# Performance work log

Measured on AMD Instinct MI355X. Metric: run time of the kernel, lower is better.

The kernel has to match this reference:

```python
import jax, jax.numpy as jnp
import numpy as np

HEAD_SIZE = 128
N_EMBD = 64
B, T = 8, 4096


def setup_inputs() -> dict:
    key = jax.random.key(0)
    k1, k2, k3, k4 = jax.random.split(key, 4)
    x = jax.random.normal(k1, (B, T, N_EMBD), dtype=jnp.float32)
    Wq = jax.random.normal(k2, (N_EMBD, HEAD_SIZE), dtype=jnp.float32) * (N_EMBD ** -0.5)
    Wk = jax.random.normal(k3, (N_EMBD, HEAD_SIZE), dtype=jnp.float32) * (N_EMBD ** -0.5)
    Wv = jax.random.normal(k4, (N_EMBD, HEAD_SIZE), dtype=jnp.float32) * (N_EMBD ** -0.5)
    return {"x": x, "Wq": Wq, "Wk": Wk, "Wv": Wv}


def reference(x, Wq, Wk, Wv):
    # x: [B, T, C]; single-head causal self-attention (nanoGPT Head)
    q = x @ Wq  # [B, T, H]
    k = x @ Wk  # [B, T, H]
    v = x @ Wv  # [B, T, H]
    scale = HEAD_SIZE ** -0.5
    scores = jnp.einsum("bth,bsh->bts", q, k) * scale  # [B, T, T]
    t = x.shape[1]
    causal = jnp.tril(jnp.ones((t, t), dtype=bool))  # [T, T]
    scores = jnp.where(causal[None, :, :], scores, jnp.float32(-jnp.inf))
    wei = jax.nn.softmax(scores, axis=-1)  # [B, T, T]; dropout p=0.0 -> identity
    out = jnp.einsum("bts,bsh->bth", wei, v)  # [B, T, H]
    return out
```

## Files before the change

### kernel.cpp

```cpp
#include <hip/hip_runtime.h>
#include <math.h>

#define BB 8
#define TT 4096
#define CC 64
#define HH 128
#define NTH 256
#define XSTR 72
#define WSTR 72
#define QSCALE ((float)(0.08838834764831845 * 1.4426950408889634))

typedef __attribute__((ext_vector_type(8)))  short short8;
typedef __attribute__((ext_vector_type(4)))  float floatx4;
typedef __attribute__((ext_vector_type(16))) float floatx16;

__device__ __forceinline__ unsigned short f2bf(float f) {
    union { float f; unsigned int u; } un; un.f = f;
    unsigned int r = un.u + 0x7FFF + ((un.u >> 16) & 1);
    return (unsigned short)(r >> 16);
}
__device__ __forceinline__ unsigned int pack2bf_fast(float a, float b) {
    union { float f; unsigned int u; } ua, ub; ua.f = a; ub.f = b;
    return __builtin_amdgcn_perm(ub.u + 0x8000u, ua.u + 0x8000u, 0x07060302u);
}
__device__ __forceinline__ float bflo(unsigned int u) {
    union { unsigned int u; float f; } x; x.u = u << 16; return x.f;
}
__device__ __forceinline__ float bfhi(unsigned int u) {
    union { unsigned int u; float f; } x; x.u = u & 0xffff0000u; return x.f;
}

__global__ __launch_bounds__(NTH) void qkv_mfma(
    const float* __restrict__ x,
    const float* __restrict__ Wq, const float* __restrict__ Wk, const float* __restrict__ Wv,
    unsigned short* __restrict__ qb, unsigned short* __restrict__ Kf,
    unsigned short* __restrict__ Vf)
{
    __shared__ __align__(16) unsigned short xs[64 * XSTR];
    __shared__ __align__(16) unsigned short Wts[3 * HH * WSTR];

    const int tid  = threadIdx.x;
    const int w    = tid >> 6;
    const int lane = tid & 63;
    const int quad = lane >> 4;
    const int lr   = lane & 15;

    const int b    = blockIdx.x >> 6;
    const int kblk = blockIdx.x & 63;
    const int t0   = kblk * 64;
    const long long rbase = (long long)b * TT + t0;

#pragma unroll
    for (int i = 0; i < 4; ++i) {
        const int idx = tid + i * NTH;
        const int r = idx >> 4, c4 = idx & 15;
        const float4 v = *(const float4*)(x + (rbase + r) * CC + c4 * 4);
        unsigned short tmp[4] = { f2bf(v.x), f2bf(v.y), f2bf(v.z), f2bf(v.w) };
        *(unsigned long long*)&xs[r * XSTR + c4 * 4] = *(unsigned long long*)tmp;
    }
#pragma unroll
    for (int mat = 0; mat < 3; ++mat) {
        const float* W = mat == 0 ? Wq : (mat == 1 ? Wk : Wv);
        const float s = mat == 0 ? QSCALE : 1.0f;
#pragma unroll
        for (int i = 0; i < 32; ++i) {
            const int idx = tid + i * NTH;
            const int c = idx >> 7, h = idx & 127;
            Wts[(mat * HH + h) * WSTR + c] = f2bf(W[idx] * s);
        }
    }
    __syncthreads();

    const short8 bx0 = *(const short8*)&xs[(w * 16 + lr) * XSTR + quad * 8];
    const short8 bx1 = *(const short8*)&xs[(w * 16 + lr) * XSTR + 32 + quad * 8];

    {
        const unsigned short* Wrow = Wts;
#pragma unroll
        for (int ht = 0; ht < 8; ++ht) {
            const short8 aw0 = *(const short8*)(Wrow + (ht * 16 + lr) * WSTR + quad * 8);
            const short8 aw1 = *(const short8*)(Wrow + (ht * 16 + lr) * WSTR + 32 + quad * 8);
            floatx4 acc = (floatx4)0.f;
            acc = __builtin_amdgcn_mfma_f32_16x16x32_bf16(aw0, bx0, acc, 0, 0, 0);
            acc = __builtin_amdgcn_mfma_f32_16x16x32_bf16(aw1, bx1, acc, 0, 0, 0);
            ushort4 st = { f2bf(acc[0]), f2bf(acc[1]), f2bf(acc[2]), f2bf(acc[3]) };
            *(ushort4*)(qb + (rbase + w * 16 + lr) * HH + ht * 16 + quad * 4) = st;
        }
    }
    {
        const unsigned short* Wrow = Wts + 1 * HH * WSTR;
        const int khp = w >> 1;
        const int lqp = (w & 1) * 16 + lr;
        unsigned short* kdst = Kf + ((long long)((b * 64 + kblk) * 2 + khp)) * 4096
                             + ((quad >> 1) & 1) * 256 + lqp * 8 + (quad & 1) * 4;
#pragma unroll
        for (int ht = 0; ht < 8; ++ht) {
            const short8 aw0 = *(const short8*)(Wrow + (ht * 16 + lr) * WSTR + quad * 8);
            const short8 aw1 = *(const short8*)(Wrow + (ht * 16 + lr) * WSTR + 32 + quad * 8);
            floatx4 acc = (floatx4)0.f;
            acc = __builtin_amdgcn_mfma_f32_16x16x32_bf16(aw0, bx0, acc, 0, 0, 0);
            acc = __builtin_amdgcn_mfma_f32_16x16x32_bf16(aw1, bx1, acc, 0, 0, 0);
            ushort4 st = { f2bf(acc[0]), f2bf(acc[1]), f2bf(acc[2]), f2bf(acc[3]) };
            *(ushort4*)(kdst + ht * 512) = st;
        }
    }
    {
        const unsigned short* Wrow = Wts + 2 * HH * WSTR;
        const int khv = w >> 1, ksv = w & 1, lsv = (quad >> 1) & 1;
        unsigned short* vdst = Vf + (long long)(b * 64 + kblk) * 8192 + khv * 4096
                             + ksv * 512 + lsv * 256 + (quad & 1) * 4;
#pragma unroll
        for (int htp = 0; htp < 8; ++htp) {
            const short8 bw0 = *(const short8*)(Wrow + (htp * 16 + lr) * WSTR + quad * 8);
            const short8 bw1 = *(const short8*)(Wrow + (htp * 16 + lr) * WSTR + 32 + quad * 8);
            floatx4 acc = (floatx4)0.f;
            acc = __builtin_amdgcn_mfma_f32_16x16x32_bf16(bx0, bw0, acc, 0, 0, 0);
            acc = __builtin_amdgcn_mfma_f32_16x16x32_bf16(bx1, bw1, acc, 0, 0, 0);
            ushort4 st = { f2bf(acc[0]), f2bf(acc[1]), f2bf(acc[2]), f2bf(acc[3]) };
            *(ushort4*)(vdst + (htp >> 1) * 1024 + ((htp & 1) * 16 + lr) * 8) = st;
        }
    }
}

__global__ __launch_bounds__(NTH, 3) void flash_splitk(
    const unsigned short* __restrict__ qb,
    const unsigned short* __restrict__ Kf,
    const unsigned short* __restrict__ Vf,
    unsigned short* __restrict__ Ob, float* __restrict__ Lb)
{
    __shared__ __align__(16) float ex[2][64 * 68];
    __shared__ float Lx[4][32];

    const int tid  = threadIdx.x;
    const int w    = tid >> 6;
    const int lane = tid & 63;
    const int lq   = lane & 31;
    const int ls   = lane >> 5;
    const int kh   = w & 1;
    const int qh   = w >> 1;

    const int id  = blockIdx.x;
    const int b   = id & 7;
    const int c   = (id >> 3) & 3;
    const int qt  = 63 - (id >> 5);
    const int len = (qt + 4) >> 2;
    const int lo  = c * len;
    if (lo > qt) return;
    const int hi  = (lo + len - 1 < qt) ? (lo + len - 1) : qt;

    const int q0 = qt * 64;
    const long long baset = (long long)b * TT;

    const unsigned short* kptr = Kf + ((long long)(b * 128 + kh)) * 4096 + lane * 8;
    const unsigned short* vptr = Vf + ((long long)b * 64) * 8192 + kh * 4096 + lane * 8;

    short8 aq[8];
    {
        const unsigned short* qrp = qb + (baset + q0 + qh * 32 + lq) * HH + ls * 8;
#pragma unroll
        for (int st = 0; st < 8; ++st)
            aq[st] = *(const short8*)(qrp + st * 16);
    }

    floatx16 o_acc[4];
#pragma unroll
    for (int ht = 0; ht < 4; ++ht) o_acc[ht] = (floatx16)0.f;
    float l_lane = 0.f;

    for (int kt = lo; kt <= hi; ++kt) {
        const unsigned short* kp = kptr + (long long)kt * 8192;
        const unsigned short* vp = vptr + (long long)kt * 8192;

        const bool diag = (kt == qt);
        if (diag && kh > qh) continue;

        short8 kfr[8], vfr[8];
#pragma unroll
        for (int st = 0; st < 8; ++st)
            kfr[st] = *(const short8*)(kp + st * 512);
#pragma unroll
        for (int i = 0; i < 8; ++i)
            vfr[i] = *(const short8*)(vp + (i >> 1) * 1024 + (i & 1) * 512);

        floatx16 s_acc = (floatx16)0.f;
#pragma unroll
        for (int st = 0; st < 8; ++st)
            s_acc = __builtin_amdgcn_mfma_f32_32x32x16_bf16(kfr[st], aq[st], s_acc, 0, 0, 0);

        float p[16];
        if (diag && kh == qh) {
#pragma unroll
            for (int reg = 0; reg < 16; ++reg) {
                const int kk = (reg & 3) + 8 * (reg >> 2) + 4 * ls;
                p[reg] = (kk <= lq) ? __builtin_amdgcn_exp2f(s_acc[reg]) : 0.f;
            }
        } else {
#pragma unroll
            for (int reg = 0; reg < 16; ++reg)
                p[reg] = __builtin_amdgcn_exp2f(s_acc[reg]);
        }
#pragma unroll
        for (int reg = 0; reg < 16; ++reg) l_lane += p[reg];

        unsigned int g[8], pg[8];
#pragma unroll
        for (int i = 0; i < 8; ++i) g[i] = pack2bf_fast(p[2 * i], p[2 * i + 1]);
#pragma unroll
        for (int i = 0; i < 8; ++i) pg[i] = __shfl_xor((int)g[i], 32);
        short8 bp[2];
#pragma unroll
        for (int ks = 0; ks < 2; ++ks) {
            union { short8 s; unsigned int u[4]; } fr;
            const int bs = ks * 4;
            if (ls == 0) {
                fr.u[0] = g[bs];      fr.u[1] = g[bs + 1];
                fr.u[2] = pg[bs];     fr.u[3] = pg[bs + 1];
            } else {
                fr.u[0] = pg[bs + 2]; fr.u[1] = pg[bs + 3];
                fr.u[2] = g[bs + 2];  fr.u[3] = g[bs + 3];
            }
            bp[ks] = fr.s;
        }

#pragma unroll
        for (int ht = 0; ht < 4; ++ht) {
            o_acc[ht] = __builtin_amdgcn_mfma_f32_32x32x16_bf16(vfr[ht * 2 + 0], bp[0], o_acc[ht], 0, 0, 0);
            o_acc[ht] = __builtin_amdgcn_mfma_f32_32x32x16_bf16(vfr[ht * 2 + 1], bp[1], o_acc[ht], 0, 0, 0);
        }
    }

    const float l2 = l_lane + __shfl_xor(l_lane, 32);
    if (lane < 32) Lx[w][lq] = l2;
    if (kh == 1) {
        float* e = &ex[qh][lane * 68];
#pragma unroll
        for (int ht = 0; ht < 4; ++ht)
#pragma unroll
            for (int rg = 0; rg < 4; ++rg) {
                float4 v = make_float4(o_acc[ht][rg * 4 + 0], o_acc[ht][rg * 4 + 1],
                                       o_acc[ht][rg * 4 + 2], o_acc[ht][rg * 4 + 3]);
                *(float4*)&e[ht * 16 + rg * 4] = v;
            }
    }
    __syncthreads();
    if (kh == 0) {
        const int pid = ((b * 64 + qt) << 2) + c;
        Lb[pid * 64 + qh * 32 + lq] = Lx[2 * qh][lq] + Lx[2 * qh + 1][lq];
        const float* e = &ex[qh][lane * 68];
        unsigned short* od = Ob + (long long)pid * 8192 + (qh * 32 + lq) * HH;
#pragma unroll
        for (int ht = 0; ht < 4; ++ht)
#pragma unroll
            for (int rg = 0; rg < 4; ++rg) {
                const float4 pv = *(const float4*)&e[ht * 16 + rg * 4];
                uint2 st;
                st.x = pack2bf_fast(o_acc[ht][rg * 4 + 0] + pv.x, o_acc[ht][rg * 4 + 1] + pv.y);
                st.y = pack2bf_fast(o_acc[ht][rg * 4 + 2] + pv.z, o_acc[ht][rg * 4 + 3] + pv.w);
                *(uint2*)(od + ht * 32 + rg * 8 + 4 * ls) = st;
            }
    }
}

__global__ __launch_bounds__(NTH) void combine(
    const unsigned short* __restrict__ Ob, const float* __restrict__ Lb,
    float* __restrict__ out)
{
    const int id = blockIdx.x;
    const int b = id & 7, qt = id >> 3;
    const int len = (qt + 4) >> 2;
    const int tid = threadIdx.x;
    const int q = tid >> 2;
    const int hg = tid & 3;
    const int pid0 = (b * 64 + qt) << 2;

    float acc[32];
#pragma unroll
    for (int i = 0; i < 32; ++i) acc[i] = 0.f;
    float ltot = 0.f;

#pragma unroll
    for (int c = 0; c < 4; ++c) {
        if (c * len > qt) break;
        ltot += Lb[(pid0 + c) * 64 + q];
        const uint4* src = (const uint4*)(Ob + (long long)(pid0 + c) * 8192 + q * HH + hg * 32);
#pragma unroll
        for (int g = 0; g < 4; ++g) {
            const uint4 d = src[g];
            acc[g * 8 + 0] += bflo(d.x); acc[g * 8 + 1] += bfhi(d.x);
            acc[g * 8 + 2] += bflo(d.y); acc[g * 8 + 3] += bfhi(d.y);
            acc[g * 8 + 4] += bflo(d.z); acc[g * 8 + 5] += bfhi(d.z);
            acc[g * 8 + 6] += bflo(d.w); acc[g * 8 + 7] += bfhi(d.w);
        }
    }
    const float inv = 1.f / ltot;
    float* op = out + ((long long)b * TT + qt * 64 + q) * HH + hg * 32;
#pragma unroll
    for (int g = 0; g < 8; ++g) {
        float4 st = make_float4(acc[g * 4 + 0] * inv, acc[g * 4 + 1] * inv,
                                acc[g * 4 + 2] * inv, acc[g * 4 + 3] * inv);
        *(float4*)(op + g * 4) = st;
    }
}

extern "C" void kernel_launch(void* const* d_in, const int* in_sizes, int n_in,
                              void* d_out, int out_size, void* d_ws, size_t ws_size,
                              hipStream_t stream)
{
    const float* x  = (const float*)d_in[0];
    const float* Wq = (const float*)d_in[1];
    const float* Wk = (const float*)d_in[2];
    const float* Wv = (const float*)d_in[3];
    float* out = (float*)d_out;

    const long long n = (long long)BB * TT * HH;
    unsigned short* qb = (unsigned short*)d_ws;
    unsigned short* Kf = qb + n;
    unsigned short* Vf = Kf + n;
    unsigned short* Ob = Vf + n;
    float*          Lb = (float*)(Ob + (long long)2048 * 8192);

    qkv_mfma<<<BB * (TT / 64), NTH, 0, stream>>>(x, Wq, Wk, Wv, qb, Kf, Vf);
    flash_splitk<<<2048, NTH, 0, stream>>>(qb, Kf, Vf, Ob, Lb);
    combine<<<BB * 64, NTH, 0, stream>>>(Ob, Lb, out);
}
```

Baseline: 151.6 us.

## Use 128-row query tiles with LDS double-buffered K/V via direct global-to-LDS loads

The split-K flash kernel now gives each block 128 query rows, one per warp at 32 rows each, in place of 64 rows split across key halves. K/V tiles of 32 keys are staged into a double-buffered LDS area using global_load_lds, so all four warps share one copy and the next tile loads while the current one computes. The cross-warp LDS reduction of partial outputs is removed, and the grid and combine indexing are adapted to 1024 blocks with equal-length key chunks. This cuts redundant global K/V reads, but adds a barrier per key tile and halves the block count, which may hurt load balance and latency hiding.

```diff
diff --git a/kernel.cpp b/kernel.cpp
--- a/kernel.cpp
+++ b/kernel.cpp
@@ -30,6 +30,12 @@
     union { unsigned int u; float f; } x; x.u = u & 0xffff0000u; return x.f;
 }
 
+__device__ __forceinline__ void gl_lds16(const void* g, void* l) {
+    __builtin_amdgcn_global_load_lds(
+        (const __attribute__((address_space(1))) unsigned int*)g,
+        (__attribute__((address_space(3))) unsigned int*)l, 16, 0, 0);
+}
+
 __global__ __launch_bounds__(NTH) void qkv_mfma(
     const float* __restrict__ x,
     const float* __restrict__ Wq, const float* __restrict__ Wk, const float* __restrict__ Wv,
@@ -122,41 +128,51 @@
     }
 }
 
+__device__ __forceinline__ void dma_tile32(
+    const unsigned char* __restrict__ Kj, const unsigned char* __restrict__ Vj,
+    unsigned char* buf, int w, int lane)
+{
+    const unsigned char* src;
+    unsigned char* dst;
+    if (w < 2) { src = Kj + w * 4096 + lane * 16;        dst = buf + w * 4096; }
+    else       { src = Vj + (w - 2) * 4096 + lane * 16;  dst = buf + 8192 + (w - 2) * 4096; }
+#pragma unroll
+    for (int i = 0; i < 4; ++i)
+        gl_lds16(src + i * 1024, dst + i * 1024);
+}
+
 __global__ __launch_bounds__(NTH, 3) void flash_splitk(
     const unsigned short* __restrict__ qb,
     const unsigned short* __restrict__ Kf,
     const unsigned short* __restrict__ Vf,
     unsigned short* __restrict__ Ob, float* __restrict__ Lb)
 {
-    __shared__ __align__(16) float ex[2][64 * 68];
-    __shared__ float Lx[4][32];
+    __shared__ __align__(16) unsigned char KV[2][16384];
 
     const int tid  = threadIdx.x;
     const int w    = tid >> 6;
     const int lane = tid & 63;
     const int lq   = lane & 31;
     const int ls   = lane >> 5;
-    const int kh   = w & 1;
-    const int qh   = w >> 1;
-
-    const int id  = blockIdx.x;
-    const int b   = id & 7;
-    const int c   = (id >> 3) & 3;
-    const int qt  = 63 - (id >> 5);
-    const int len = (qt + 4) >> 2;
+
+    const int id = blockIdx.x;
+    const int b  = id & 7;
+    const int c  = (id >> 3) & 3;
+    const int qt = 31 - (id >> 5);
+    const int len = qt + 1;
     const int lo  = c * len;
-    if (lo > qt) return;
-    const int hi  = (lo + len - 1 < qt) ? (lo + len - 1) : qt;
-
-    const int q0 = qt * 64;
+    const int hi  = lo + qt;
+
+    const int q0 = qt * 128;
     const long long baset = (long long)b * TT;
-
-    const unsigned short* kptr = Kf + ((long long)(b * 128 + kh)) * 4096 + lane * 8;
-    const unsigned short* vptr = Vf + ((long long)b * 64) * 8192 + kh * 4096 + lane * 8;
+    const unsigned char* Kbase = (const unsigned char*)Kf + (long long)b * 128 * 8192;
+    const unsigned char* Vbase = (const unsigned char*)Vf + (long long)b * 128 * 8192;
+
+    dma_tile32(Kbase + (long long)lo * 8192, Vbase + (long long)lo * 8192, KV[0], w, lane);
 
     short8 aq[8];
     {
-        const unsigned short* qrp = qb + (baset + q0 + qh * 32 + lq) * HH + ls * 8;
+        const unsigned short* qrp = qb + (baset + q0 + w * 32 + lq) * HH + ls * 8;
 #pragma unroll
         for (int st = 0; st < 8; ++st)
             aq[st] = *(const short8*)(qrp + st * 16);
@@ -167,98 +183,88 @@
     for (int ht = 0; ht < 4; ++ht) o_acc[ht] = (floatx16)0.f;
     float l_lane = 0.f;
 
-    for (int kt = lo; kt <= hi; ++kt) {
-        const unsigned short* kp = kptr + (long long)kt * 8192;
-        const unsigned short* vp = vptr + (long long)kt * 8192;
-
-        const bool diag = (kt == qt);
-        if (diag && kh > qh) continue;
-
-        short8 kfr[8], vfr[8];
-#pragma unroll
-        for (int st = 0; st < 8; ++st)
-            kfr[st] = *(const short8*)(kp + st * 512);
-#pragma unroll
-        for (int i = 0; i < 8; ++i)
-            vfr[i] = *(const short8*)(vp + (i >> 1) * 1024 + (i & 1) * 512);
-
-        floatx16 s_acc = (floatx16)0.f;
-#pragma unroll
-        for (int st = 0; st < 8; ++st)
-            s_acc = __builtin_amdgcn_mfma_f32_32x32x16_bf16(kfr[st], aq[st], s_acc, 0, 0, 0);
-
-        float p[16];
-        if (diag && kh == qh) {
-#pragma unroll
-            for (int reg = 0; reg < 16; ++reg) {
-                const int kk = (reg & 3) + 8 * (reg >> 2) + 4 * ls;
-                p[reg] = (kk <= lq) ? __builtin_amdgcn_exp2f(s_acc[reg]) : 0.f;
+    for (int j = lo; j <= hi; ++j) {
+        const int cb = (j - lo) & 1;
+        __syncthreads();
+        if (j < hi)
+            dma_tile32(Kbase + (long long)(j + 1) * 8192, Vbase + (long long)(j + 1) * 8192,
+                       KV[cb ^ 1], w, lane);
+
+        const int D = q0 + w * 32 - j * 32;
+        if (D > -32) {
+            const unsigned short* Kt = (const unsigned short*)&KV[cb][0];
+            const unsigned short* Vt = (const unsigned short*)&KV[cb][8192];
+
+            short8 kfr[8], vfr[8];
+#pragma unroll
+            for (int st = 0; st < 8; ++st)
+                kfr[st] = *(const short8*)(Kt + st * 512 + lane * 8);
+#pragma unroll
+            for (int i = 0; i < 8; ++i)
+                vfr[i] = *(const short8*)(Vt + (i >> 1) * 1024 + (i & 1) * 512 + lane * 8);
+
+            floatx16 s_acc = (floatx16)0.f;
+#pragma unroll
+            for (int st = 0; st < 8; ++st)
+                s_acc = __builtin_amdgcn_mfma_f32_32x32x16_bf16(kfr[st], aq[st], s_acc, 0, 0, 0);
+
+            float p[16];
+            if (D < 31) {
+#pragma unroll
+                for (int reg = 0; reg < 16; ++reg) {
+                    const int kk = (reg & 3) + 8 * (reg >> 2) + 4 * ls;
+                    p[reg] = (kk <= lq + D) ? __builtin_amdgcn_exp2f(s_acc[reg]) : 0.f;
+                }
+            } else {
+#pragma unroll
+                for (int reg = 0; reg < 16; ++reg)
+                    p[reg] = __builtin_amdgcn_exp2f(s_acc[reg]);
             }
-        } else {
-#pragma unroll
-            for (int reg = 0; reg < 16; ++reg)
-                p[reg] = __builtin_amdgcn_exp2f(s_acc[reg]);
-        }
-#pragma unroll
-        for (int reg = 0; reg < 16; ++reg) l_lane += p[reg];
-
-        unsigned int g[8], pg[8];
-#pragma unroll
-        for (int i = 0; i < 8; ++i) g[i] = pack2bf_fast(p[2 * i], p[2 * i + 1]);
-#pragma unroll
-        for (int i = 0; i < 8; ++i) pg[i] = __shfl_xor((int)g[i], 32);
-        short8 bp[2];
-#pragma unroll
-        for (int ks = 0; ks < 2; ++ks) {
-            union { short8 s; unsigned int u[4]; } fr;
-            const int bs = ks * 4;
-            if (ls == 0) {
-                fr.u[0] = g[bs];      fr.u[1] = g[bs + 1];
-                fr.u[2] = pg[bs];     fr.u[3] = pg[bs + 1];
-            } else {
-                fr.u[0] = pg[bs + 2]; fr.u[1] = pg[bs + 3];
-                fr.u[2] = g[bs + 2];  fr.u[3] = g[bs + 3];
+#pragma unroll
+            for (int reg = 0; reg < 16; ++reg) l_lane += p[reg];
+
+            unsigned int g[8], pg[8];
+#pragma unroll
+            for (int i = 0; i < 8; ++i) g[i] = pack2bf_fast(p[2 * i], p[2 * i + 1]);
+#pragma unroll
+            for (int i = 0; i < 8; ++i) pg[i] = __shfl_xor((int)g[i], 32);
+            short8 bp[2];
+#pragma unroll
+            for (int ks = 0; ks < 2; ++ks) {
+                union { short8 s; unsigned int u[4]; } fr;
+                const int bs = ks * 4;
+                if (ls == 0) {
+                    fr.u[0] = g[bs];      fr.u[1] = g[bs + 1];
+                    fr.u[2] = pg[bs];     fr.u[3] = pg[bs + 1];
+                } else {
+                    fr.u[0] = pg[bs + 2]; fr.u[1] = pg[bs + 3];
+                    fr.u[2] = g[bs + 2];  fr.u[3] = g[bs + 3];
+                }
+                bp[ks] = fr.s;
             }
-            bp[ks] = fr.s;
-        }
-
-#pragma unroll
-        for (int ht = 0; ht < 4; ++ht) {
-            o_acc[ht] = __builtin_amdgcn_mfma_f32_32x32x16_bf16(vfr[ht * 2 + 0], bp[0], o_acc[ht], 0, 0, 0);
-            o_acc[ht] = __builtin_amdgcn_mfma_f32_32x32x16_bf16(vfr[ht * 2 + 1], bp[1], o_acc[ht], 0, 0, 0);
-        }
-    }
-
+
+#pragma unroll
+            for (int ht = 0; ht < 4; ++ht) {
+                o_acc[ht] = __builtin_amdgcn_mfma_f32_32x32x16_bf16(vfr[ht * 2 + 0], bp[0], o_acc[ht], 0, 0, 0);
+                o_acc[ht] = __builtin_amdgcn_mfma_f32_32x32x16_bf16(vfr[ht * 2 + 1], bp[1], o_acc[ht], 0, 0, 0);
+            }
+        }
+    }
+
+    const int pid = ((b * 32 + qt) << 2) + c;
     const float l2 = l_lane + __shfl_xor(l_lane, 32);
-    if (lane < 32) Lx[w][lq] = l2;
-    if (kh == 1) {
-        float* e = &ex[qh][lane * 68];
-#pragma unroll
-        for (int ht = 0; ht < 4; ++ht)
-#pragma unroll
-            for (int rg = 0; rg < 4; ++rg) {
-                float4 v = make_float4(o_acc[ht][rg * 4 + 0], o_acc[ht][rg * 4 + 1],
-                                       o_acc[ht][rg * 4 + 2], o_acc[ht][rg * 4 + 3]);
-                *(float4*)&e[ht * 16 + rg * 4] = v;
-            }
-    }
-    __syncthreads();
-    if (kh == 0) {
-        const int pid = ((b * 64 + qt) << 2) + c;
-        Lb[pid * 64 + qh * 32 + lq] = Lx[2 * qh][lq] + Lx[2 * qh + 1][lq];
-        const float* e = &ex[qh][lane * 68];
-        unsigned short* od = Ob + (long long)pid * 8192 + (qh * 32 + lq) * HH;
-#pragma unroll
-        for (int ht = 0; ht < 4; ++ht)
-#pragma unroll
-            for (int rg = 0; rg < 4; ++rg) {
-                const float4 pv = *(const float4*)&e[ht * 16 + rg * 4];
-                uint2 st;
-                st.x = pack2bf_fast(o_acc[ht][rg * 4 + 0] + pv.x, o_acc[ht][rg * 4 + 1] + pv.y);
-                st.y = pack2bf_fast(o_acc[ht][rg * 4 + 2] + pv.z, o_acc[ht][rg * 4 + 3] + pv.w);
-                *(uint2*)(od + ht * 32 + rg * 8 + 4 * ls) = st;
-            }
-    }
+    if (lane < 32) Lb[pid * 128 + w * 32 + lq] = l2;
+
+    unsigned short* od = Ob + (long long)pid * 16384 + (w * 32 + lq) * HH;
+#pragma unroll
+    for (int ht = 0; ht < 4; ++ht)
+#pragma unroll
+        for (int rg = 0; rg < 4; ++rg) {
+            uint2 st;
+            st.x = pack2bf_fast(o_acc[ht][rg * 4 + 0], o_acc[ht][rg * 4 + 1]);
+            st.y = pack2bf_fast(o_acc[ht][rg * 4 + 2], o_acc[ht][rg * 4 + 3]);
+            *(uint2*)(od + ht * 32 + rg * 8 + 4 * ls) = st;
+        }
 }
 
 __global__ __launch_bounds__(NTH) void combine(
@@ -266,12 +272,13 @@
     float* __restrict__ out)
 {
     const int id = blockIdx.x;
-    const int b = id & 7, qt = id >> 3;
-    const int len = (qt + 4) >> 2;
+    const int b = id & 7;
+    const int rest = id >> 3;
+    const int qt = rest >> 1, half = rest & 1;
     const int tid = threadIdx.x;
-    const int q = tid >> 2;
+    const int q = half * 64 + (tid >> 2);
     const int hg = tid & 3;
-    const int pid0 = (b * 64 + qt) << 2;
+    const int pid0 = ((b * 32 + qt) << 2);
 
     float acc[32];
 #pragma unroll
@@ -280,9 +287,8 @@
 
 #pragma unroll
     for (int c = 0; c < 4; ++c) {
-        if (c * len > qt) break;
-        ltot += Lb[(pid0 + c) * 64 + q];
-        const uint4* src = (const uint4*)(Ob + (long long)(pid0 + c) * 8192 + q * HH + hg * 32);
+        ltot += Lb[(pid0 + c) * 128 + q];
+        const uint4* src = (const uint4*)(Ob + (long long)(pid0 + c) * 16384 + q * HH + hg * 32);
 #pragma unroll
         for (int g = 0; g < 4; ++g) {
             const uint4 d = src[g];
@@ -293,7 +299,7 @@
         }
     }
     const float inv = 1.f / ltot;
-    float* op = out + ((long long)b * TT + qt * 64 + q) * HH + hg * 32;
+    float* op = out + ((long long)b * TT + qt * 128 + q) * HH + hg * 32;
 #pragma unroll
     for (int g = 0; g < 8; ++g) {
         float4 st = make_float4(acc[g * 4 + 0] * inv, acc[g * 4 + 1] * inv,
@@ -317,9 +323,9 @@
     unsigned short* Kf = qb + n;
     unsigned short* Vf = Kf + n;
     unsigned short* Ob = Vf + n;
-    float*          Lb = (float*)(Ob + (long long)2048 * 8192);
+    float*          Lb = (float*)(Ob + (long long)1024 * 16384);
 
     qkv_mfma<<<BB * (TT / 64), NTH, 0, stream>>>(x, Wq, Wk, Wv, qb, Kf, Vf);
-    flash_splitk<<<2048, NTH, 0, stream>>>(qb, Kf, Vf, Ob, Lb);
+    flash_splitk<<<1024, NTH, 0, stream>>>(qb, Kf, Vf, Ob, Lb);
     combine<<<BB * 64, NTH, 0, stream>>>(Ob, Lb, out);
 }
```

New measurement: 144.0 us. 5.0% less time.
